# Kernel optimization log

Measured on AMD Instinct MI355X. Metric: run time of the kernel, lower is better.

Reference implementation:

```python
import jax, jax.numpy as jnp
import numpy as np

B, T, Z, AE, H, M, A = 32, 512, 128, 16, 1024, 5, 18
OUT = Z * 3 * M + 1  # 1921
K = M * Z  # per-component split size for logmix/mu/logstd


def setup_inputs() -> dict:
    key = jax.random.key(0)
    ks = jax.random.split(key, 9)
    s = 0.02
    return {
        "z": jax.random.normal(ks[0], (B, T, Z), jnp.float32),
        "actions": jax.random.randint(ks[1], (B, T), 0, A, jnp.int32),
        "dones": jax.random.randint(ks[2], (B, T), 0, 2, jnp.int32),
        "embed": jax.random.normal(ks[3], (A, AE), jnp.float32) * s,
        "W_ih": jax.random.normal(ks[4], (4 * H, Z + AE), jnp.float32) * s,
        "W_hh": jax.random.normal(ks[5], (4 * H, H), jnp.float32) * s,
        "b_ih": jnp.zeros((4 * H,), jnp.float32),
        "b_hh": jnp.zeros((4 * H,), jnp.float32),
        "W_out": jax.random.normal(ks[6], (OUT, H), jnp.float32) * s,
        "b_out": jnp.zeros((OUT,), jnp.float32),
    }


def reference(z, actions, dones, embed, W_ih, W_hh, b_ih, b_hh, W_out, b_out):
    a_emb = embed[actions]                              # [B,T,AE]
    inp = jnp.concatenate([z, a_emb], axis=2)           # [B,T,Z+AE]
    d = dones.astype(inp.dtype)                         # [B,T]
    # precompute input contribution to gates for all timesteps (one big GEMM)
    x_pre = jnp.einsum('btf,gf->btg', inp, W_ih) + b_ih + b_hh  # [B,T,4H]

    def cell(carry, xt):
        h, c = carry
        xg, dt = xt                                     # xg: [B,4H], dt: [B]
        gates = xg + h @ W_hh.T
        i, f, g, o = jnp.split(gates, 4, axis=1)        # torch LSTMCell order i,f,g,o
        c_new = jax.nn.sigmoid(f) * c + jax.nn.sigmoid(i) * jnp.tanh(g)
        h_new = jax.nn.sigmoid(o) * jnp.tanh(c_new)
        mask = (1.0 - dt)[:, None]                      # done-masking AFTER output
        return (h_new * mask, c_new * mask), h_new

    h0 = jnp.zeros((B, H), inp.dtype)
    _, hs = jax.lax.scan(cell, (h0, h0), (x_pre.transpose(1, 0, 2), d.T))
    hs = hs.transpose(1, 0, 2)[:, :-1]                  # [B,T-1,H]
    out = hs @ W_out.T + b_out                          # [B,T-1,OUT]

    logmix = out[..., :K].reshape(-1, M)
    mu = out[..., K:2 * K].reshape(-1, M)
    logstd = out[..., 2 * K:3 * K].reshape(-1, M)
    done_p = out[..., 3 * K:].squeeze(-1)               # [B,T-1]
    logmix = logmix - jax.scipy.special.logsumexp(logmix, axis=1, keepdims=True)
    return logmix, mu, logstd, done_p
```

## Files before the change

### kernel.cpp

```cpp
#include <hip/hip_runtime.h>
#include <hip/hip_bf16.h>


typedef float f4 __attribute__((ext_vector_type(4)));
typedef short s8 __attribute__((ext_vector_type(8)));
typedef unsigned short us8v __attribute__((ext_vector_type(8)));
typedef unsigned short us4v __attribute__((ext_vector_type(4)));
typedef unsigned long long u64;
typedef unsigned u32;

#define DEV __device__ __forceinline__

DEV unsigned short f2b(float f) {
  unsigned u = __float_as_uint(f);
  return (unsigned short)((u + 0x7FFFu + ((u >> 16) & 1u)) >> 16);
}
DEV float b2f(unsigned short s) { return __uint_as_float(((unsigned)s) << 16); }

DEV f4 MFMA(s8 a, s8 b, f4 c) {
  return __builtin_amdgcn_mfma_f32_16x16x32_bf16(a, b, c, 0, 0, 0);
}
DEV s8 LD8(const unsigned short* p) { return *reinterpret_cast<const s8*>(p); }

DEV u32 AL32(const u32* p) {
  return __hip_atomic_load(p, __ATOMIC_RELAXED, __HIP_MEMORY_SCOPE_AGENT);
}
DEV void AS(u64* p, u64 v) {
  __hip_atomic_store(p, v, __ATOMIC_RELAXED, __HIP_MEMORY_SCOPE_AGENT);
}

DEV float sigf(float x) {
  float e = __builtin_amdgcn_exp2f(x * -1.44269504f);
  return __builtin_amdgcn_rcpf(1.f + e);
}
DEV float tanhf_fast(float x) {
  float e = __builtin_amdgcn_exp2f(x * 2.88539008f);
  return 1.f - 2.f * __builtin_amdgcn_rcpf(e + 1.f);
}

static constexpr size_t WS_GCNT = 0;
static constexpr size_t WS_NACT = 2048;
static constexpr size_t WS_HDR  = 4096;
static constexpr size_t WS_META = 4352;
static constexpr size_t WS_LOFF = 69888;
static constexpr size_t WS_TMP  = 131072;
static constexpr size_t WS_ZT   = 131072;
static constexpr size_t WS_WOUT = 4325376;
static constexpr size_t WS_HS2  = 8261632;
static constexpr size_t WS_END  = 41816064;
static constexpr size_t DO_CALL = 35651584;

__global__ void cvt_wout_k(const float* __restrict__ W, unsigned short* __restrict__ o) {
  int i = blockIdx.x * 256 + threadIdx.x;
  if (i < 491776) {
    const float4 v = reinterpret_cast<const float4*>(W)[i];
    us4v u; u[0] = f2b(v.x); u[1] = f2b(v.y); u[2] = f2b(v.z); u[3] = f2b(v.w);
    reinterpret_cast<us4v*>(o)[i] = u;
  }
}

__global__ void cvt_z_k(const float* __restrict__ z, unsigned short* __restrict__ zt) {
  int i = blockIdx.x * 256 + threadIdx.x;
  if (i < 524288) {
    const float4 v = reinterpret_cast<const float4*>(z)[i];
    us4v u; u[0] = f2b(v.x); u[1] = f2b(v.y); u[2] = f2b(v.z); u[3] = f2b(v.w);
    reinterpret_cast<us4v*>(zt)[i] = u;
  }
}

__global__ void zero_hs_tail_k(u64* __restrict__ hs2) {
  int i = blockIdx.x * 256 + threadIdx.x;
  if (i < 8192) {
    int region = i >> 5, r = 16352 + (i & 31);
    hs2[(size_t)region * 16384 + r] = 0ull;
  }
}

__global__ __launch_bounds__(256) void seg_build_k(
    const int* __restrict__ dones, u32* __restrict__ tmp,
    u32* __restrict__ meta, u32* __restrict__ nact, u32* __restrict__ hdr,
    u32* __restrict__ loff) {
  __shared__ u32 hist[512];
  __shared__ u32 cur[512];
  __shared__ u32 scnt[32];
  const int tid = threadIdx.x;
  for (int i = tid; i < 512; i += 256) hist[i] = 0;
  __syncthreads();
  if (tid < 32) {
    int b = tid, cnt = 0, t0 = 0;
    for (int t = 1; t <= 511; ++t) {
      bool brk = (t == 511) || (dones[b * 512 + t - 1] != 0);
      if (brk) {
        int len = t - t0;
        tmp[b * 511 + cnt] = ((u32)t0 << 16) | (u32)len;
        atomicAdd(&hist[len], 1u);
        ++cnt; t0 = t;
      }
    }
    scnt[b] = (u32)cnt;
  }
  __syncthreads();
  if (tid == 0) {
    u32 acc = 0; int ml = 0;
    for (int L = 511; L >= 0; --L) {
      cur[L] = acc; nact[L] = acc;
      if (hist[L] && !ml) ml = L;
      acc += hist[L];
    }
    hdr[0] = acc; hdr[1] = (u32)ml;
    u32 off = 0; loff[0] = 0;
    for (int s2 = 1; s2 <= ml; ++s2) { loff[s2] = off; off += nact[s2]; }
  }
  __syncthreads();
  if (tid < 32) {
    int b = tid; u32 c = scnt[b];
    for (u32 i = 0; i < c; ++i) {
      u32 e = tmp[b * 511 + i];
      u32 len = e & 0xFFFFu, t0 = e >> 16;
      u32 slot = atomicAdd(&cur[len], 1u);
      meta[slot] = ((u32)b << 20) | (t0 << 10) | len;
    }
  }
}

__global__ __launch_bounds__(1024, 1) void lstm_seg_k(
    const float* __restrict__ Whh, const float* __restrict__ Wih,
    const float* __restrict__ embed, const float* __restrict__ bih,
    const float* __restrict__ bhh, const int* __restrict__ actions,
    const unsigned short* __restrict__ zt, const u32* __restrict__ meta,
    const u32* __restrict__ nact, const u32* __restrict__ hdr,
    const u32* __restrict__ loff, u64* __restrict__ hsl,
    u64* __restrict__ c_all, u64* __restrict__ hs2,
    u32* __restrict__ gcnt) {
  const int blk = blockIdx.x;
  const int tid = threadIdx.x;
  const int lane = tid & 63;
  const int w = tid >> 6;
  const int ln = lane & 15, lk = lane >> 4;

  __shared__ alignas(16) unsigned short whh_sw[32 * 64 * 8];
  __shared__ alignas(16) unsigned short wz_sw[4 * 64 * 8];
  __shared__ float abias[18][16];
  __shared__ float red[16][64][17];

  for (int i = tid; i < 32 * 64 * 8; i += 1024) {
    int j = i & 7, L = (i >> 3) & 63, kt = i >> 9;
    int n = L & 15;
    int grow = (n >> 2) * 1024 + blk * 4 + (n & 3);
    int k = kt * 32 + ((L >> 4) << 3) + j;
    whh_sw[i] = f2b(Whh[grow * 1024 + k]);
  }
  for (int i = tid; i < 4 * 64 * 8; i += 1024) {
    int j = i & 7, L = (i >> 3) & 63, kt = i >> 9;
    int n = L & 15;
    int grow = (n >> 2) * 1024 + blk * 4 + (n & 3);
    int k = kt * 32 + ((L >> 4) << 3) + j;
    wz_sw[i] = f2b(Wih[grow * 144 + k]);
  }
  for (int i = tid; i < 18 * 16; i += 1024) {
    int a = i >> 4, n = i & 15;
    int grow = (n >> 2) * 1024 + blk * 4 + (n & 3);
    float s = bih[grow] + bhh[grow];
    for (int j = 0; j < 16; ++j) s += embed[a * 16 + j] * Wih[grow * 144 + 128 + j];
    abias[a][n] = s;
  }
  __syncthreads();

  const int maxlen = (int)hdr[1];

  for (int s = 0; s < maxlen; ++s) {
    const u32 N = nact[s];
    const int ntiles = (int)((N + 63) >> 6);
    const u64* hread = hsl + (size_t)loff[s] * 256;
    u64* hwrite = hsl + (size_t)loff[s + 1] * 256;

    for (int tile = w; tile < ntiles; tile += 16) {
      const u32 sb = (u32)tile << 6;
      const u32 slot = sb + (u32)lane;
      const bool valid = slot < N;
      const u32 m = valid ? meta[slot] : 0u;
      const u32 b = m >> 20, t0 = (m >> 10) & 1023u, L = m & 1023u;
      const int zrow = (int)(b * 512u + t0 + (u32)s);
      const int orow = (int)(b * 511u + t0 + (u32)s);
      const u32 act = valid ? (u32)actions[zrow] : 0u;
      union { u64 q[2]; } cc; cc.q[0] = 0; cc.q[1] = 0;
      if (s && valid) {
        const u64* cp = c_all + ((size_t)blk << 14) + ((size_t)slot << 1);
        cc.q[0] = cp[0]; cc.q[1] = cp[1];
      }
      int zr[4];
#pragma unroll
      for (int q = 0; q < 4; ++q) zr[q] = __shfl(zrow, ln + 16 * q, 64);

      f4 acc0 = {0.f,0.f,0.f,0.f}, acc1 = {0.f,0.f,0.f,0.f};
      f4 acc2 = {0.f,0.f,0.f,0.f}, acc3 = {0.f,0.f,0.f,0.f};
#pragma unroll
      for (int kz = 0; kz < 4; ++kz) {
        s8 bf = LD8(wz_sw + ((kz * 64 + lane) << 3));
        s8 a0 = LD8(zt + (size_t)zr[0] * 128 + kz * 32 + (lk << 3));
        s8 a1 = LD8(zt + (size_t)zr[1] * 128 + kz * 32 + (lk << 3));
        s8 a2 = LD8(zt + (size_t)zr[2] * 128 + kz * 32 + (lk << 3));
        s8 a3 = LD8(zt + (size_t)zr[3] * 128 + kz * 32 + (lk << 3));
        acc0 = MFMA(a0, bf, acc0);  acc1 = MFMA(a1, bf, acc1);
        acc2 = MFMA(a2, bf, acc2);  acc3 = MFMA(a3, bf, acc3);
      }
      if (s) {
        const u32 r0c = (sb + (u32)ln      < N) ? sb + (u32)ln      : N - 1u;
        const u32 r1c = (sb + (u32)ln + 16 < N) ? sb + (u32)ln + 16 : N - 1u;
        const u32 r2c = (sb + (u32)ln + 32 < N) ? sb + (u32)ln + 32 : N - 1u;
        const u32 r3c = (sb + (u32)ln + 48 < N) ? sb + (u32)ln + 48 : N - 1u;
        const unsigned short* h0 =
            (const unsigned short*)(hread + (size_t)r0c * 256) + (lk << 3);
        const unsigned short* h1 =
            (const unsigned short*)(hread + (size_t)r1c * 256) + (lk << 3);
        const unsigned short* h2 =
            (const unsigned short*)(hread + (size_t)r2c * 256) + (lk << 3);
        const unsigned short* h3 =
            (const unsigned short*)(hread + (size_t)r3c * 256) + (lk << 3);
#pragma unroll 8
        for (int kt = 0; kt < 32; ++kt) {
          s8 bf = LD8(whh_sw + ((kt * 64 + lane) << 3));
          s8 f0 = LD8(h0 + (kt << 5));
          s8 f1 = LD8(h1 + (kt << 5));
          s8 f2 = LD8(h2 + (kt << 5));
          s8 f3 = LD8(h3 + (kt << 5));
          acc0 = MFMA(f0, bf, acc0);  acc1 = MFMA(f1, bf, acc1);
          acc2 = MFMA(f2, bf, acc2);  acc3 = MFMA(f3, bf, acc3);
        }
      }

#pragma unroll
      for (int j = 0; j < 4; ++j) {
        red[w][(lk << 2) + j][ln]      = acc0[j];
        red[w][16 + (lk << 2) + j][ln] = acc1[j];
        red[w][32 + (lk << 2) + j][ln] = acc2[j];
        red[w][48 + (lk << 2) + j][ln] = acc3[j];
      }
      const bool carry = valid && (L > (u32)(s + 1));
      u32 cb[4]; unsigned short hb[4];
#pragma unroll
      for (int e = 0; e < 4; ++e) {
        float gi = red[w][lane][e]      + abias[act][e];
        float gf = red[w][lane][4 + e]  + abias[act][4 + e];
        float gg = red[w][lane][8 + e]  + abias[act][8 + e];
        float go = red[w][lane][12 + e] + abias[act][12 + e];
        const u32 cpb = (e == 0) ? (u32)cc.q[0] : (e == 1) ? (u32)(cc.q[0] >> 32)
                       : (e == 2) ? (u32)cc.q[1] : (u32)(cc.q[1] >> 32);
        const float cprev = __uint_as_float(cpb);
        const float si = sigf(gi), sf = sigf(gf), so = sigf(go);
        const float cn = sf * cprev + si * tanhf_fast(gg);
        const float hn = so * tanhf_fast(cn);
        cb[e] = __float_as_uint(cn);
        hb[e] = f2b(hn);
      }
      if (carry) {
        u64* cp = c_all + ((size_t)blk << 14) + ((size_t)slot << 1);
        cp[0] = ((u64)cb[1] << 32) | (u64)cb[0];
        cp[1] = ((u64)cb[3] << 32) | (u64)cb[2];
      }
      const u64 hu = (u64)hb[0] | ((u64)hb[1] << 16) |
                     ((u64)hb[2] << 32) | ((u64)hb[3] << 48);
      if (valid) {
        hs2[((size_t)blk << 14) + orow] = hu;
        if (carry) AS(hwrite + (size_t)slot * 256 + blk, hu);
      }
    }

    asm volatile("s_waitcnt vmcnt(0)" ::: "memory");
    __syncthreads();
    if (s + 1 < maxlen) {
      if (tid == 0) {
        __hip_atomic_fetch_add(gcnt + (blk >> 4) * 32, 1u,
                               __ATOMIC_RELAXED, __HIP_MEMORY_SCOPE_AGENT);
        const u32 tgt = (u32)(s + 1) * 16u;
        for (u32 spin = 0; spin < (1u << 20); ++spin) {
          u32 mn = 0xFFFFFFFFu;
#pragma unroll
          for (int g = 0; g < 16; ++g) {
            u32 v = AL32(gcnt + g * 32);
            mn = (v < mn) ? v : mn;
          }
          if (mn >= tgt) break;
          __builtin_amdgcn_s_sleep(1);
        }
      }
      __syncthreads();
    }
  }
}

__global__ __launch_bounds__(256, 2) void out_gemm_k(
    const u64* __restrict__ hs2, const unsigned short* __restrict__ wout,
    const float* __restrict__ b_out, float* __restrict__ out) {
  const int mblk = blockIdx.x, nblk = blockIdx.y;
  const int tid = threadIdx.x, lane = tid & 63, w = tid >> 6;
  const int ln = lane & 15, lk = lane >> 4;
  __shared__ alignas(16) unsigned char smraw[26112];
  unsigned short* bsm = (unsigned short*)smraw;
  float* ep = (float*)smraw;
  const bool last = (nblk == 23);

  if (last) {
    for (int i = tid; i < 15 * 136; i += 256) bsm[81 * 136 + i] = 0;
  }
  __syncthreads();

  const int r0 = mblk * 64 + w * 16;
  f4 acc[5];
#pragma unroll
  for (int s = 0; s < 5; ++s) acc[s] = (f4){0.f, 0.f, 0.f, 0.f};
  f4 acc5 = {0.f, 0.f, 0.f, 0.f};

  for (int kc = 0; kc < 8; ++kc) {
#pragma unroll
    for (int ii = 0; ii < 5; ++ii) {
      int i = tid + ii * 256;
      int n = i >> 4, k16 = i & 15;
      us8v v = *reinterpret_cast<const us8v*>(
          wout + (size_t)(nblk * 80 + n) * 1024 + kc * 128 + (k16 << 3));
      *reinterpret_cast<us8v*>(bsm + n * 136 + (k16 << 3)) = v;
    }
    if (last && tid < 16) {
      us8v v = *reinterpret_cast<const us8v*>(
          wout + (size_t)1920 * 1024 + kc * 128 + (tid << 3));
      *reinterpret_cast<us8v*>(bsm + 80 * 136 + (tid << 3)) = v;
    }
    __syncthreads();
#pragma unroll
    for (int ks = 0; ks < 4; ++ks) {
      const int k0 = kc * 128 + ks * 32 + (lk << 3);
      union { u64 q[2]; s8 v; } ua;
      ua.q[0] = hs2[(size_t)(k0 >> 2) * 16384 + r0 + ln];
      ua.q[1] = hs2[((size_t)(k0 >> 2) + 1) * 16384 + r0 + ln];
#pragma unroll
      for (int s = 0; s < 5; ++s) {
        s8 b = LD8(bsm + (s * 16 + ln) * 136 + ks * 32 + (lk << 3));
        acc[s] = MFMA(ua.v, b, acc[s]);
      }
      if (last) {
        s8 b6 = LD8(bsm + ((80 + ln) * 136) + ks * 32 + (lk << 3));
        acc5 = MFMA(ua.v, b6, acc5);
      }
    }
    __syncthreads();
  }

  const int T = nblk >> 3;
  if (T) {
    float* base = out + (size_t)10465280 * T;
    const int lc0 = (nblk - (T << 3)) * 80;
#pragma unroll
    for (int s = 0; s < 5; ++s) {
      const int lc = lc0 + s * 16 + ln;
      const float bias = b_out[T * 640 + lc];
#pragma unroll
      for (int j = 0; j < 4; ++j) {
        const int row = r0 + (lk << 2) + j;
        if (row < 16352) base[(size_t)row * 640 + lc] = acc[s][j] + bias;
      }
    }
    if (last && ln == 0) {
      const float bias = b_out[1920];
#pragma unroll
      for (int j = 0; j < 4; ++j) {
        const int row = r0 + (lk << 2) + j;
        if (row < 16352) out[31395840 + row] = acc5[j] + bias;
      }
    }
  } else {
#pragma unroll
    for (int s = 0; s < 5; ++s) {
      const float bias = b_out[nblk * 80 + s * 16 + ln];
#pragma unroll
      for (int j = 0; j < 4; ++j)
        ep[(w * 16 + (lk << 2) + j) * 84 + s * 16 + ln] = acc[s][j] + bias;
    }
    __syncthreads();
    for (int task = tid; task < 1024; task += 256) {
      const int rr = task >> 4, grp = task & 15;
      const int row = mblk * 64 + rr;
      const float* e = ep + rr * 84 + grp * 5;
      float v0 = e[0], v1 = e[1], v2 = e[2], v3 = e[3], v4 = e[4];
      float mx = fmaxf(fmaxf(fmaxf(v0, v1), fmaxf(v2, v3)), v4);
      float ssum = expf(v0 - mx) + expf(v1 - mx) + expf(v2 - mx) +
                   expf(v3 - mx) + expf(v4 - mx);
      float lse = mx + logf(ssum);
      if (row < 16352) {
        float* o = out + (size_t)row * 640 + nblk * 80 + grp * 5;
        o[0] = v0 - lse; o[1] = v1 - lse; o[2] = v2 - lse;
        o[3] = v3 - lse; o[4] = v4 - lse;
      }
    }
  }
}

extern "C" void kernel_launch(void* const* d_in, const int* in_sizes, int n_in,
                              void* d_out, int out_size, void* d_ws, size_t ws_size,
                              hipStream_t stream) {
  const float* z       = (const float*)d_in[0];
  const int*   actions = (const int*)d_in[1];
  const int*   dones   = (const int*)d_in[2];
  const float* embed   = (const float*)d_in[3];
  const float* Wih     = (const float*)d_in[4];
  const float* Whh     = (const float*)d_in[5];
  const float* bih     = (const float*)d_in[6];
  const float* bhh     = (const float*)d_in[7];
  const float* Wout    = (const float*)d_in[8];
  const float* bout    = (const float*)d_in[9];
  float* out = (float*)d_out;

  if (ws_size < WS_END) return;

  char* ws = (char*)d_ws;
  u32* gcnt              = (u32*)(ws + WS_GCNT);
  u32* nact              = (u32*)(ws + WS_NACT);
  u32* hdr               = (u32*)(ws + WS_HDR);
  u32* metaA             = (u32*)(ws + WS_META);
  u32* loff              = (u32*)(ws + WS_LOFF);
  u32* tmp               = (u32*)(ws + WS_TMP);
  unsigned short* zt     = (unsigned short*)(ws + WS_ZT);
  unsigned short* wout16 = (unsigned short*)(ws + WS_WOUT);
  u64* hs2               = (u64*)(ws + WS_HS2);
  u64* hsl   = (u64*)d_out;
  u64* call  = (u64*)((char*)d_out + DO_CALL);

  hipMemsetAsync(d_ws, 0, 2048, stream);

  seg_build_k<<<1, 256, 0, stream>>>(dones, tmp, metaA, nact, hdr, loff);
  cvt_z_k<<<2048, 256, 0, stream>>>(z, zt);
  zero_hs_tail_k<<<32, 256, 0, stream>>>(hs2);
  lstm_seg_k<<<256, 1024, 0, stream>>>(Whh, Wih, embed, bih, bhh, actions,
                                       zt, metaA, nact, hdr, loff, hsl, call,
                                       hs2, gcnt);
  cvt_wout_k<<<1921, 256, 0, stream>>>(Wout, wout16);
  out_gemm_k<<<dim3(256, 24), 256, 0, stream>>>(hs2, wout16, bout, out);
}
```

Measured before the change: 1.036 ms.

## Give each LSTM block 8 hidden units and split row tiles across block pairs

Each block of the persistent LSTM kernel now owns 8 hidden units (32 gate columns) rather than 4. Pairs of blocks share the same units and split the batch-row tiles between them, with 512 threads per block instead of 1024. Each h fragment loaded from global memory now feeds two MFMAs, roughly halving h-read traffic per unit of work, at the cost of doubling the W_hh slice kept in LDS. The hs2 layout is changed so each row's 8 hidden values are contiguous, and the output GEMM reads a single 16-byte vector instead of two 8-byte loads.

```diff
diff --git a/kernel.cpp b/kernel.cpp
--- a/kernel.cpp
+++ b/kernel.cpp
@@ -71,8 +71,8 @@
 __global__ void zero_hs_tail_k(u64* __restrict__ hs2) {
   int i = blockIdx.x * 256 + threadIdx.x;
   if (i < 8192) {
-    int region = i >> 5, r = 16352 + (i & 31);
-    hs2[(size_t)region * 16384 + r] = 0ull;
+    int region = i >> 6, rr = (i & 63) >> 1, hf = i & 1;
+    hs2[((size_t)region * 16384 + 16352 + rr) * 2 + hf] = 0ull;
   }
 }
 
@@ -123,7 +123,7 @@
   }
 }
 
-__global__ __launch_bounds__(1024, 1) void lstm_seg_k(
+__global__ __launch_bounds__(512, 1) void lstm_seg_k(
     const float* __restrict__ Whh, const float* __restrict__ Wih,
     const float* __restrict__ embed, const float* __restrict__ bih,
     const float* __restrict__ bhh, const int* __restrict__ actions,
@@ -133,33 +133,35 @@
     u64* __restrict__ c_all, u64* __restrict__ hs2,
     u32* __restrict__ gcnt) {
   const int blk = blockIdx.x;
+  const int g = blk >> 1;
+  const int half = blk & 1;
   const int tid = threadIdx.x;
   const int lane = tid & 63;
   const int w = tid >> 6;
   const int ln = lane & 15, lk = lane >> 4;
 
-  __shared__ alignas(16) unsigned short whh_sw[32 * 64 * 8];
-  __shared__ alignas(16) unsigned short wz_sw[4 * 64 * 8];
-  __shared__ float abias[18][16];
-  __shared__ float red[16][64][17];
-
-  for (int i = tid; i < 32 * 64 * 8; i += 1024) {
-    int j = i & 7, L = (i >> 3) & 63, kt = i >> 9;
-    int n = L & 15;
-    int grow = (n >> 2) * 1024 + blk * 4 + (n & 3);
+  __shared__ alignas(16) unsigned short whh_sw[32 * 2 * 64 * 8];
+  __shared__ alignas(16) unsigned short wz_sw[4 * 2 * 64 * 8];
+  __shared__ float abias[18][32];
+  __shared__ float red[8][64][33];
+
+  for (int i = tid; i < 32768; i += 512) {
+    int j = i & 7, L = (i >> 3) & 63, nt = (i >> 9) & 1, kt = i >> 10;
+    int n = nt * 16 + (L & 15);
+    int grow = (n >> 3) * 1024 + g * 8 + (n & 7);
     int k = kt * 32 + ((L >> 4) << 3) + j;
     whh_sw[i] = f2b(Whh[grow * 1024 + k]);
   }
-  for (int i = tid; i < 4 * 64 * 8; i += 1024) {
-    int j = i & 7, L = (i >> 3) & 63, kt = i >> 9;
-    int n = L & 15;
-    int grow = (n >> 2) * 1024 + blk * 4 + (n & 3);
-    int k = kt * 32 + ((L >> 4) << 3) + j;
+  for (int i = tid; i < 4096; i += 512) {
+    int j = i & 7, L = (i >> 3) & 63, nt = (i >> 9) & 1, kz = i >> 10;
+    int n = nt * 16 + (L & 15);
+    int grow = (n >> 3) * 1024 + g * 8 + (n & 7);
+    int k = kz * 32 + ((L >> 4) << 3) + j;
     wz_sw[i] = f2b(Wih[grow * 144 + k]);
   }
-  for (int i = tid; i < 18 * 16; i += 1024) {
-    int a = i >> 4, n = i & 15;
-    int grow = (n >> 2) * 1024 + blk * 4 + (n & 3);
+  for (int i = tid; i < 18 * 32; i += 512) {
+    int a = i >> 5, n = i & 31;
+    int grow = (n >> 3) * 1024 + g * 8 + (n & 7);
     float s = bih[grow] + bhh[grow];
     for (int j = 0; j < 16; ++j) s += embed[a * 16 + j] * Wih[grow * 144 + 128 + j];
     abias[a][n] = s;
@@ -174,7 +176,7 @@
     const u64* hread = hsl + (size_t)loff[s] * 256;
     u64* hwrite = hsl + (size_t)loff[s + 1] * 256;
 
-    for (int tile = w; tile < ntiles; tile += 16) {
+    for (int tile = half + 2 * w; tile < ntiles; tile += 16) {
       const u32 sb = (u32)tile << 6;
       const u32 slot = sb + (u32)lane;
       const bool valid = slot < N;
@@ -183,26 +185,29 @@
       const int zrow = (int)(b * 512u + t0 + (u32)s);
       const int orow = (int)(b * 511u + t0 + (u32)s);
       const u32 act = valid ? (u32)actions[zrow] : 0u;
-      union { u64 q[2]; } cc; cc.q[0] = 0; cc.q[1] = 0;
+      u64 cq[4] = {0, 0, 0, 0};
       if (s && valid) {
-        const u64* cp = c_all + ((size_t)blk << 14) + ((size_t)slot << 1);
-        cc.q[0] = cp[0]; cc.q[1] = cp[1];
+        const u64* cp = c_all + ((size_t)blk << 15) + ((size_t)slot << 2);
+        cq[0] = cp[0]; cq[1] = cp[1]; cq[2] = cp[2]; cq[3] = cp[3];
       }
       int zr[4];
 #pragma unroll
       for (int q = 0; q < 4; ++q) zr[q] = __shfl(zrow, ln + 16 * q, 64);
 
-      f4 acc0 = {0.f,0.f,0.f,0.f}, acc1 = {0.f,0.f,0.f,0.f};
-      f4 acc2 = {0.f,0.f,0.f,0.f}, acc3 = {0.f,0.f,0.f,0.f};
+      f4 a00 = {0,0,0,0}, a01 = {0,0,0,0}, a10 = {0,0,0,0}, a11 = {0,0,0,0};
+      f4 a20 = {0,0,0,0}, a21 = {0,0,0,0}, a30 = {0,0,0,0}, a31 = {0,0,0,0};
 #pragma unroll
       for (int kz = 0; kz < 4; ++kz) {
-        s8 bf = LD8(wz_sw + ((kz * 64 + lane) << 3));
-        s8 a0 = LD8(zt + (size_t)zr[0] * 128 + kz * 32 + (lk << 3));
-        s8 a1 = LD8(zt + (size_t)zr[1] * 128 + kz * 32 + (lk << 3));
-        s8 a2 = LD8(zt + (size_t)zr[2] * 128 + kz * 32 + (lk << 3));
-        s8 a3 = LD8(zt + (size_t)zr[3] * 128 + kz * 32 + (lk << 3));
-        acc0 = MFMA(a0, bf, acc0);  acc1 = MFMA(a1, bf, acc1);
-        acc2 = MFMA(a2, bf, acc2);  acc3 = MFMA(a3, bf, acc3);
+        s8 b0 = LD8(wz_sw + (((kz * 2 + 0) * 64 + lane) << 3));
+        s8 b1 = LD8(wz_sw + (((kz * 2 + 1) * 64 + lane) << 3));
+        s8 f0 = LD8(zt + (size_t)zr[0] * 128 + kz * 32 + (lk << 3));
+        s8 f1 = LD8(zt + (size_t)zr[1] * 128 + kz * 32 + (lk << 3));
+        s8 f2 = LD8(zt + (size_t)zr[2] * 128 + kz * 32 + (lk << 3));
+        s8 f3 = LD8(zt + (size_t)zr[3] * 128 + kz * 32 + (lk << 3));
+        a00 = MFMA(f0, b0, a00);  a01 = MFMA(f0, b1, a01);
+        a10 = MFMA(f1, b0, a10);  a11 = MFMA(f1, b1, a11);
+        a20 = MFMA(f2, b0, a20);  a21 = MFMA(f2, b1, a21);
+        a30 = MFMA(f3, b0, a30);  a31 = MFMA(f3, b1, a31);
       }
       if (s) {
         const u32 r0c = (sb + (u32)ln      < N) ? sb + (u32)ln      : N - 1u;
@@ -219,33 +224,39 @@
             (const unsigned short*)(hread + (size_t)r3c * 256) + (lk << 3);
 #pragma unroll 8
         for (int kt = 0; kt < 32; ++kt) {
-          s8 bf = LD8(whh_sw + ((kt * 64 + lane) << 3));
+          s8 b0 = LD8(whh_sw + (((kt * 2 + 0) * 64 + lane) << 3));
+          s8 b1 = LD8(whh_sw + (((kt * 2 + 1) * 64 + lane) << 3));
           s8 f0 = LD8(h0 + (kt << 5));
           s8 f1 = LD8(h1 + (kt << 5));
           s8 f2 = LD8(h2 + (kt << 5));
           s8 f3 = LD8(h3 + (kt << 5));
-          acc0 = MFMA(f0, bf, acc0);  acc1 = MFMA(f1, bf, acc1);
-          acc2 = MFMA(f2, bf, acc2);  acc3 = MFMA(f3, bf, acc3);
+          a00 = MFMA(f0, b0, a00);  a01 = MFMA(f0, b1, a01);
+          a10 = MFMA(f1, b0, a10);  a11 = MFMA(f1, b1, a11);
+          a20 = MFMA(f2, b0, a20);  a21 = MFMA(f2, b1, a21);
+          a30 = MFMA(f3, b0, a30);  a31 = MFMA(f3, b1, a31);
         }
       }
 
 #pragma unroll
       for (int j = 0; j < 4; ++j) {
-        red[w][(lk << 2) + j][ln]      = acc0[j];
-        red[w][16 + (lk << 2) + j][ln] = acc1[j];
-        red[w][32 + (lk << 2) + j][ln] = acc2[j];
-        red[w][48 + (lk << 2) + j][ln] = acc3[j];
+        red[w][(lk << 2) + j][ln]           = a00[j];
+        red[w][(lk << 2) + j][16 + ln]      = a01[j];
+        red[w][16 + (lk << 2) + j][ln]      = a10[j];
+        red[w][16 + (lk << 2) + j][16 + ln] = a11[j];
+        red[w][32 + (lk << 2) + j][ln]      = a20[j];
+        red[w][32 + (lk << 2) + j][16 + ln] = a21[j];
+        red[w][48 + (lk << 2) + j][ln]      = a30[j];
+        red[w][48 + (lk << 2) + j][16 + ln] = a31[j];
       }
       const bool carry = valid && (L > (u32)(s + 1));
-      u32 cb[4]; unsigned short hb[4];
-#pragma unroll
-      for (int e = 0; e < 4; ++e) {
+      u32 cb[8]; unsigned short hb[8];
+#pragma unroll
+      for (int e = 0; e < 8; ++e) {
         float gi = red[w][lane][e]      + abias[act][e];
-        float gf = red[w][lane][4 + e]  + abias[act][4 + e];
-        float gg = red[w][lane][8 + e]  + abias[act][8 + e];
-        float go = red[w][lane][12 + e] + abias[act][12 + e];
-        const u32 cpb = (e == 0) ? (u32)cc.q[0] : (e == 1) ? (u32)(cc.q[0] >> 32)
-                       : (e == 2) ? (u32)cc.q[1] : (u32)(cc.q[1] >> 32);
+        float gf = red[w][lane][8 + e]  + abias[act][8 + e];
+        float gg = red[w][lane][16 + e] + abias[act][16 + e];
+        float go = red[w][lane][24 + e] + abias[act][24 + e];
+        const u32 cpb = (e & 1) ? (u32)(cq[e >> 1] >> 32) : (u32)cq[e >> 1];
         const float cprev = __uint_as_float(cpb);
         const float si = sigf(gi), sf = sigf(gf), so = sigf(go);
         const float cn = sf * cprev + si * tanhf_fast(gg);
@@ -254,15 +265,23 @@
         hb[e] = f2b(hn);
       }
       if (carry) {
-        u64* cp = c_all + ((size_t)blk << 14) + ((size_t)slot << 1);
+        u64* cp = c_all + ((size_t)blk << 15) + ((size_t)slot << 2);
         cp[0] = ((u64)cb[1] << 32) | (u64)cb[0];
         cp[1] = ((u64)cb[3] << 32) | (u64)cb[2];
-      }
-      const u64 hu = (u64)hb[0] | ((u64)hb[1] << 16) |
-                     ((u64)hb[2] << 32) | ((u64)hb[3] << 48);
+        cp[2] = ((u64)cb[5] << 32) | (u64)cb[4];
+        cp[3] = ((u64)cb[7] << 32) | (u64)cb[6];
+      }
+      const u64 hu0 = (u64)hb[0] | ((u64)hb[1] << 16) |
+                      ((u64)hb[2] << 32) | ((u64)hb[3] << 48);
+      const u64 hu1 = (u64)hb[4] | ((u64)hb[5] << 16) |
+                      ((u64)hb[6] << 32) | ((u64)hb[7] << 48);
       if (valid) {
-        hs2[((size_t)blk << 14) + orow] = hu;
-        if (carry) AS(hwrite + (size_t)slot * 256 + blk, hu);
+        u64* hp = hs2 + ((size_t)g * 16384 + orow) * 2;
+        hp[0] = hu0; hp[1] = hu1;
+        if (carry) {
+          AS(hwrite + (size_t)slot * 256 + 2 * g, hu0);
+          AS(hwrite + (size_t)slot * 256 + 2 * g + 1, hu1);
+        }
       }
     }
 
@@ -276,8 +295,8 @@
         for (u32 spin = 0; spin < (1u << 20); ++spin) {
           u32 mn = 0xFFFFFFFFu;
 #pragma unroll
-          for (int g = 0; g < 16; ++g) {
-            u32 v = AL32(gcnt + g * 32);
+          for (int gg2 = 0; gg2 < 16; ++gg2) {
+            u32 v = AL32(gcnt + gg2 * 32);
             mn = (v < mn) ? v : mn;
           }
           if (mn >= tgt) break;
@@ -329,17 +348,16 @@
 #pragma unroll
     for (int ks = 0; ks < 4; ++ks) {
       const int k0 = kc * 128 + ks * 32 + (lk << 3);
-      union { u64 q[2]; s8 v; } ua;
-      ua.q[0] = hs2[(size_t)(k0 >> 2) * 16384 + r0 + ln];
-      ua.q[1] = hs2[((size_t)(k0 >> 2) + 1) * 16384 + r0 + ln];
+      s8 a = *reinterpret_cast<const s8*>(
+          hs2 + ((size_t)(k0 >> 3) * 16384 + r0 + ln) * 2);
 #pragma unroll
       for (int s = 0; s < 5; ++s) {
         s8 b = LD8(bsm + (s * 16 + ln) * 136 + ks * 32 + (lk << 3));
-        acc[s] = MFMA(ua.v, b, acc[s]);
+        acc[s] = MFMA(a, b, acc[s]);
       }
       if (last) {
         s8 b6 = LD8(bsm + ((80 + ln) * 136) + ks * 32 + (lk << 3));
-        acc5 = MFMA(ua.v, b6, acc5);
+        acc5 = MFMA(a, b6, acc5);
       }
     }
     __syncthreads();
@@ -429,9 +447,9 @@
   seg_build_k<<<1, 256, 0, stream>>>(dones, tmp, metaA, nact, hdr, loff);
   cvt_z_k<<<2048, 256, 0, stream>>>(z, zt);
   zero_hs_tail_k<<<32, 256, 0, stream>>>(hs2);
-  lstm_seg_k<<<256, 1024, 0, stream>>>(Whh, Wih, embed, bih, bhh, actions,
-                                       zt, metaA, nact, hdr, loff, hsl, call,
-                                       hs2, gcnt);
+  lstm_seg_k<<<256, 512, 0, stream>>>(Whh, Wih, embed, bih, bhh, actions,
+                                      zt, metaA, nact, hdr, loff, hsl, call,
+                                      hs2, gcnt);
   cvt_wout_k<<<1921, 256, 0, stream>>>(Wout, wout16);
   out_gemm_k<<<dim3(256, 24), 256, 0, stream>>>(hs2, wout16, bout, out);
 }
```

Measured after the change: 863.6 us. 1.2x faster.
